# Kernel optimization log

Hardware: AMD Instinct MI355X
Metric: run time of the kernel (lower is better)

The kernel has to match this reference:

```python
import jax, jax.numpy as jnp
import numpy as np
import math

DIM = 2048
D_STATE = 64
EXPAND = 2
CHUNK = 64
HEADDIM = 64
D_CONV = 4
D_INNER = EXPAND * DIM          # 4096
NHEADS = D_INNER // HEADDIM     # 64


def _segsum(x):
    """x: (..., T) -> (..., T, T); out[i,j] = sum_{k=j+1}^{i} x[k] for i>=j else -inf."""
    T = x.shape[-1]
    keep = jnp.tril(jnp.ones((T, T), bool), -1)          # strictly lower
    seg = jnp.cumsum(jnp.where(keep, x[..., None], 0.0), axis=-2)
    valid = jnp.tril(jnp.ones((T, T), bool))
    return jnp.where(valid, seg, -jnp.inf)


def _ssd(X, A, B, C, block):
    """Chunkwise SSD scan (Mamba-2 Listing 1). X:(b,L,h,p) A:(b,L,h) B,C:(b,L,h,n)."""
    b, L, h, p = X.shape
    n = B.shape[-1]
    c = L // block
    X = X.reshape(b, c, block, h, p)
    A = A.reshape(b, c, block, h)
    B = B.reshape(b, c, block, h, n)
    C = C.reshape(b, c, block, h, n)
    A = jnp.transpose(A, (0, 3, 1, 2))                    # (b,h,c,l)
    A_cum = jnp.cumsum(A, axis=-1)
    # intra-chunk (diagonal block) output
    L_intra = jnp.exp(_segsum(A))                         # (b,h,c,l,s)
    Y_diag = jnp.einsum('bclhn,bcshn,bhcls,bcshp->bclhp', C, B, L_intra, X)
    # per-chunk final states
    decay_states = jnp.exp(A_cum[..., -1:] - A_cum)       # (b,h,c,l)
    states = jnp.einsum('bclhn,bhcl,bclhp->bchpn', B, decay_states, X)
    states = jnp.concatenate([jnp.zeros_like(states[:, :1]), states], axis=1)
    # inter-chunk recurrence across chunk boundaries
    chunk_end = jnp.pad(A_cum[..., -1], ((0, 0), (0, 0), (1, 0)))  # (b,h,c+1)
    decay_chunk = jnp.exp(_segsum(chunk_end))             # (b,h,c+1,c+1)
    new_states = jnp.einsum('bhzc,bchpn->bzhpn', decay_chunk, states)
    states_per_chunk = new_states[:, :-1]
    # off-diagonal contribution from carried-in states
    state_decay_out = jnp.exp(A_cum)                      # (b,h,c,l)
    Y_off = jnp.einsum('bclhn,bchpn,bhcl->bclhp', C, states_per_chunk, state_decay_out)
    return (Y_diag + Y_off).reshape(b, L, h, p)


def setup_inputs() -> dict:
    key = jax.random.key(0)
    ks = jax.random.split(key, 6)
    b, l = 2, 2048
    x = jax.random.normal(ks[0], (b, l, DIM), jnp.float32)
    proj_out = 2 * D_INNER + 2 * D_STATE + NHEADS
    in_proj_w = jax.random.normal(ks[1], (proj_out, DIM), jnp.float32) / math.sqrt(DIM)
    conv_w = jax.random.normal(ks[2], (D_INNER, 1, D_CONV), jnp.float32) / math.sqrt(D_CONV)
    conv_b = jnp.zeros((D_INNER,), jnp.float32)
    out_proj_w = jax.random.normal(ks[3], (DIM, D_INNER), jnp.float32) / math.sqrt(D_INNER)
    A_log = jnp.zeros((NHEADS,), jnp.float32)
    D_skip = jnp.ones((D_INNER,), jnp.float32)
    u = jax.random.uniform(ks[4], (NHEADS,), jnp.float32)
    dt = jnp.clip(jnp.exp(u * (math.log(0.1) - math.log(0.001)) + math.log(0.001)), 1e-4, None)
    dt_bias = dt + jnp.log(-jnp.expm1(-dt))
    return dict(x=x, in_proj_w=in_proj_w, conv_w=conv_w, conv_b=conv_b,
                out_proj_w=out_proj_w, A_log=A_log, D_skip=D_skip, dt_bias=dt_bias)


def reference(x, in_proj_w, conv_w, conv_b, out_proj_w, A_log, D_skip, dt_bias):
    b, l, _ = x.shape
    proj = x @ in_proj_w.T
    splits = [D_INNER, 2 * D_INNER, 2 * D_INNER + D_STATE, 2 * D_INNER + 2 * D_STATE]
    x_branch, z, B_in, C_in, dt = jnp.split(proj, splits, axis=-1)
    # causal depthwise conv1d (torch pads both sides then slices [:l] == left-pad only)
    xc = jnp.transpose(x_branch, (0, 2, 1))               # (b, d_inner, l)
    xc = jax.lax.conv_general_dilated(
        xc, conv_w, (1,), [(D_CONV - 1, 0)],
        dimension_numbers=('NCH', 'OIH', 'NCH'), feature_group_count=D_INNER)
    xc = xc + conv_b[None, :, None]
    x_act = jax.nn.silu(jnp.transpose(xc, (0, 2, 1)))     # (b,l,d_inner)
    x_h = x_act.reshape(b, l, NHEADS, HEADDIM)
    dt_f = jax.nn.softplus(dt + dt_bias)                  # (b,l,h)
    A_f = -jnp.exp(A_log)                                 # (h,)
    X_disc = x_h * dt_f[..., None]
    A_disc = A_f[None, None, :] * dt_f
    B_b = jnp.broadcast_to(B_in[:, :, None, :], (b, l, NHEADS, D_STATE))
    C_b = jnp.broadcast_to(C_in[:, :, None, :], (b, l, NHEADS, D_STATE))
    Y = _ssd(X_disc, A_disc, B_b, C_b, CHUNK)             # (b,l,h,p)
    y = Y.reshape(b, l, D_INNER) + D_skip * x_act
    y = y * jax.nn.silu(z)
    return y @ out_proj_w.T
```

## Files before the change

kernel.cpp:

```cpp
#include <hip/hip_runtime.h>

typedef unsigned short u16;
typedef unsigned int   u32;
typedef __attribute__((ext_vector_type(8))) short bf16x8;
typedef __attribute__((ext_vector_type(4))) float f32x4;

__device__ __forceinline__ u16 f2bf(float f){
  u32 u = __builtin_bit_cast(u32, f);
  u32 r = (u + 0x7FFFu + ((u >> 16) & 1u)) >> 16;
  return (u16)r;
}
__device__ __forceinline__ float bf2f(u16 h){
  u32 u = ((u32)h) << 16;
  return __builtin_bit_cast(float, u);
}
__device__ __forceinline__ void llds16(const u16* g, u16* l){
  __builtin_amdgcn_global_load_lds((const __attribute__((address_space(1))) void*)g,
                                   (__attribute__((address_space(3))) void*)l, 16, 0, 0);
}

__global__ __launch_bounds__(256) void cast4(const float* __restrict__ in, u16* __restrict__ out, int n4){
  int i = blockIdx.x * 256 + threadIdx.x;
  if (i >= n4) return;
  float4 v = ((const float4*)in)[i];
  u32 lo = (u32)f2bf(v.x) | ((u32)f2bf(v.y) << 16);
  u32 hi = (u32)f2bf(v.z) | ((u32)f2bf(v.w) << 16);
  ((uint2*)out)[i] = make_uint2(lo, hi);
}

__global__ __launch_bounds__(256) void castpad_w1(const float* __restrict__ in, u16* __restrict__ out){
  int i = blockIdx.x * 256 + threadIdx.x;
  if (i >= 8448 * 512) return;
  int nrow = i >> 9;
  float4 v = make_float4(0.f, 0.f, 0.f, 0.f);
  if (nrow < 8384) v = ((const float4*)in)[i];
  u32 lo = (u32)f2bf(v.x) | ((u32)f2bf(v.y) << 16);
  u32 hi = (u32)f2bf(v.z) | ((u32)f2bf(v.w) << 16);
  ((uint2*)out)[i] = make_uint2(lo, hi);
}

template<bool OUTF32>
__global__ __launch_bounds__(256)
void gemm128(const u16* __restrict__ A, const u16* __restrict__ Bm, void* __restrict__ Cout,
             int NYT, int N, int K)
{
  __shared__ u16 As[8192], Bs[8192];
  const int tid = threadIdx.x;
  const int lane = tid & 63, wave = tid >> 6;
  const int wm = (wave >> 1) * 64, wn = (wave & 1) * 64;
  const int lr = lane & 15, lk8 = (lane >> 4) * 8;
  const int lterm = lr * 32 + (lk8 ^ ((lr & 8) << 1));
  const int nwg = gridDim.x;
  const int lid = blockIdx.x;
  const int q = nwg >> 3;
  const int swz = (lid & 7) * q + (lid >> 3);
  const int ty = swz % NYT, tx = swz / NYT;
  const size_t bm0 = (size_t)ty * 128;
  const size_t bn0 = (size_t)tx * 128;
  const int cg = (lane & 3) ^ ((lane & 32) ? 2 : 0);
  const int rsub = lane >> 2;
  const int ag0 = (wave >> 1) * 8;
  const int bg0 = (wave & 1) * 8;

  f32x4 acc[4][4] = {};

  for (int k0 = 0; k0 < K; k0 += 64) {
    __syncthreads();
    #pragma unroll
    for (int u = 0; u < 4; u++) {
      const int si = wave * 4 + u;
      const int row = (si >> 1) * 16 + rsub;
      const int kc = (si & 1) * 32 + cg * 8;
      llds16(A  + (bm0 + row) * (size_t)K + k0 + kc, As + si * 512 + lane * 8);
      llds16(Bm + (bn0 + row) * (size_t)K + k0 + kc, Bs + si * 512 + lane * 8);
    }
    __syncthreads();
    #pragma unroll
    for (int kb = 0; kb < 2; kb++) {
      bf16x8 af[4], bfv[4];
      #pragma unroll
      for (int m = 0; m < 4; m++) af[m]  = *(const bf16x8*)&As[(ag0 + m * 2 + kb) * 512 + lterm];
      #pragma unroll
      for (int n = 0; n < 4; n++) bfv[n] = *(const bf16x8*)&Bs[(bg0 + n * 2 + kb) * 512 + lterm];
      #pragma unroll
      for (int m = 0; m < 4; m++)
        #pragma unroll
        for (int n = 0; n < 4; n++)
          acc[m][n] = __builtin_amdgcn_mfma_f32_16x16x32_bf16(af[m], bfv[n], acc[m][n], 0, 0, 0);
    }
  }

  const int lg = (lane >> 4) * 4;
  #pragma unroll
  for (int m = 0; m < 4; m++)
    #pragma unroll
    for (int n = 0; n < 4; n++) {
      size_t col = bn0 + wn + n * 16 + lr;
      #pragma unroll
      for (int j = 0; j < 4; j++) {
        size_t row = bm0 + wm + m * 16 + lg + j;
        float v = acc[m][n][j];
        if (OUTF32) ((float*)Cout)[row * N + col] = v;
        else        ((u16*)Cout)[row * N + col] = f2bf(v);
      }
    }
}

__global__ __launch_bounds__(256)
void postproj(const u16* __restrict__ proj, const float* __restrict__ dt_bias,
              float* __restrict__ dtf, u16* __restrict__ Bb, u16* __restrict__ Cb)
{
  int i = blockIdx.x * 256 + threadIdx.x;
  if (i >= 4096 * 64) return;
  int bl = i >> 6, hh = i & 63;
  const u16* pr = proj + (size_t)bl * 8448;
  float dv = bf2f(pr[8320 + hh]) + dt_bias[hh];
  dtf[i] = dv > 20.f ? dv : log1pf(__expf(dv));
  Bb[i] = pr[8192 + hh];
  Cb[i] = pr[8256 + hh];
}

__global__ __launch_bounds__(256)
void conv_silu(const u16* __restrict__ proj, const float* __restrict__ cw,
               const float* __restrict__ cb, const float* __restrict__ dtf,
               u16* __restrict__ xact, u16* __restrict__ Xd)
{
  const int g = blockIdx.x;
  const int bl0 = g * 4;
  const int l0 = bl0 & 2047;
  const int d0 = blockIdx.y * 2048 + threadIdx.x * 8;
  const int hd = d0 >> 6;
  float4 wv[8];
  #pragma unroll
  for (int e = 0; e < 8; e++) wv[e] = *(const float4*)&cw[(size_t)(d0 + e) * 4];
  float bias[8];
  {
    float4 b0 = *(const float4*)&cb[d0];
    float4 b1 = *(const float4*)&cb[d0 + 4];
    bias[0]=b0.x; bias[1]=b0.y; bias[2]=b0.z; bias[3]=b0.w;
    bias[4]=b1.x; bias[5]=b1.y; bias[6]=b1.z; bias[7]=b1.w;
  }
  float r[7][8];
  #pragma unroll
  for (int t = 0; t < 7; t++) {
    const int l = l0 - 3 + t;
    if (l >= 0) {
      uint4 rv = *(const uint4*)(proj + (size_t)(bl0 - 3 + t) * 8448 + d0);
      const u16* re = (const u16*)&rv;
      #pragma unroll
      for (int e = 0; e < 8; e++) r[t][e] = bf2f(re[e]);
    } else {
      #pragma unroll
      for (int e = 0; e < 8; e++) r[t][e] = 0.f;
    }
  }
  #pragma unroll
  for (int lo = 0; lo < 4; lo++) {
    const float dt = dtf[(size_t)(bl0 + lo) * 64 + hd];
    u16 xo[8], xdo[8];
    #pragma unroll
    for (int e = 0; e < 8; e++) {
      float v = bias[e] + wv[e].x * r[lo][e] + wv[e].y * r[lo + 1][e]
                        + wv[e].z * r[lo + 2][e] + wv[e].w * r[lo + 3][e];
      float sil = v / (1.f + __expf(-v));
      xo[e]  = f2bf(sil);
      xdo[e] = f2bf(sil * dt);
    }
    *(uint4*)(xact + (size_t)(bl0 + lo) * 4096 + d0) = *(const uint4*)xo;
    *(uint4*)(Xd   + (size_t)(bl0 + lo) * 4096 + d0) = *(const uint4*)xdo;
  }
}

__global__ __launch_bounds__(256)
void ssd_states(const u16* __restrict__ Xd, const u16* __restrict__ Bg,
                const float* __restrict__ dtf, const float* __restrict__ A_log,
                u16* __restrict__ Stg, float* __restrict__ dtot)
{
  const int wg = blockIdx.x;
  const int b = wg >> 11, h = wg & 63;
  const int c = (wg >> 6) & 31;
  const int bl0 = b * 2048 + c * 64;
  __shared__ u16 Bt[64*64], Xts[64*64];
  __shared__ float avals[64], Acum[64], Adec[64];
  const int tid = threadIdx.x, wave = tid >> 6, lane = tid & 63;
  const int qi = (wave >> 1) * 32, qj = (wave & 1) * 32;
  const int lr = lane & 15, lk8 = (lane >> 4) * 8, lg = (lane >> 4) * 4;
  const float negA = -__expf(A_log[h]);

  if (tid < 64) avals[tid] = negA * dtf[(size_t)(bl0 + tid) * 64 + h];
  __syncthreads();
  if (tid < 64) { float s = 0.f; for (int j = 0; j <= tid; j++) s += avals[j]; Acum[tid] = s; }
  __syncthreads();
  if (tid < 64) Adec[tid] = __expf(Acum[63] - Acum[tid]);
  if (tid == 0) dtot[wg] = __expf(Acum[63]);
  __syncthreads();
  {
    int s = tid & 63, c0 = (tid >> 6) * 16;
    float dec = Adec[s];
    const u16* bs = Bg + (size_t)(bl0 + s) * 64 + c0;
    const u16* xs = Xd + (size_t)(bl0 + s) * 4096 + h * 64 + c0;
    #pragma unroll
    for (int j = 0; j < 16; j++) {
      Bt[(c0 + j) * 64 + s] = bs[j];
      Xts[(c0 + j) * 64 + s] = f2bf(bf2f(xs[j]) * dec);
    }
  }
  __syncthreads();
  f32x4 accst[2][2] = {};
  #pragma unroll
  for (int kk = 0; kk < 64; kk += 32) {
    bf16x8 xsf[2], btf[2];
    #pragma unroll
    for (int t = 0; t < 2; t++) {
      xsf[t] = *(const bf16x8*)&Xts[(qi + t * 16 + lr) * 64 + kk + lk8];
      btf[t] = *(const bf16x8*)&Bt [(qj + t * 16 + lr) * 64 + kk + lk8];
    }
    #pragma unroll
    for (int ti = 0; ti < 2; ti++)
      #pragma unroll
      for (int tj = 0; tj < 2; tj++)
        accst[ti][tj] = __builtin_amdgcn_mfma_f32_16x16x32_bf16(xsf[ti], btf[tj], accst[ti][tj], 0, 0, 0);
  }
  u16* So = Stg + (size_t)wg * 4096;
  #pragma unroll
  for (int ti = 0; ti < 2; ti++)
    #pragma unroll
    for (int tj = 0; tj < 2; tj++) {
      int nn = qj + tj * 16 + lr;
      #pragma unroll
      for (int r2 = 0; r2 < 4; r2++) {
        int pp = qi + ti * 16 + lg + r2;
        So[pp * 64 + nn] = f2bf(accst[ti][tj][r2]);
      }
    }
}

__global__ __launch_bounds__(256)
void ssd_scan(u16* __restrict__ Stg, const float* __restrict__ dtot)
{
  const int gid = blockIdx.x * 256 + threadIdx.x;
  const int bh = gid >> 12;
  const int pn = gid & 4095;
  const int b = bh >> 6, h = bh & 63;
  float R = 0.f;
  for (int c = 0; c < 32; ++c) {
    const int whc = b * 2048 + c * 64 + h;
    size_t idx = (size_t)whc * 4096 + pn;
    float st = bf2f(Stg[idx]);
    Stg[idx] = f2bf(R);
    R = R * dtot[whc] + st;
  }
}

__global__ __launch_bounds__(256)
void ssd_y(const u16* __restrict__ Xd, const u16* __restrict__ Bg, const u16* __restrict__ Cg,
           const float* __restrict__ dtf, const float* __restrict__ A_log,
           const u16* __restrict__ xact, const u16* __restrict__ proj,
           const float* __restrict__ Dskip, const u16* __restrict__ Stg,
           u16* __restrict__ Yout)
{
  const int wg = blockIdx.x;
  const int b = wg >> 11, h = wg & 63;
  const int c = (wg >> 6) & 31;
  const int bl0 = b * 2048 + c * 64;
  __shared__ u16 Cb[64*64], Bb[64*64], Xt[64*64], Sb[64*64], P[64*64];
  __shared__ float avals[64], Acum[64], Aexp[64];
  const int tid = threadIdx.x, wave = tid >> 6, lane = tid & 63;
  const int qi = (wave >> 1) * 32, qj = (wave & 1) * 32;
  const int lr = lane & 15, lk8 = (lane >> 4) * 8, lg = (lane >> 4) * 4;
  const float negA = -__expf(A_log[h]);

  if (tid < 64) avals[tid] = negA * dtf[(size_t)(bl0 + tid) * 64 + h];
  __syncthreads();
  if (tid < 64) { float s = 0.f; for (int j = 0; j <= tid; j++) s += avals[j]; Acum[tid] = s; }
  __syncthreads();
  if (tid < 64) Aexp[tid] = __expf(Acum[tid]);
  __syncthreads();
  {
    int l = tid >> 2, n0 = (tid & 3) * 16;
    const uint4* s0 = (const uint4*)(Cg + (size_t)(bl0 + l) * 64 + n0);
    *(uint4*)&Cb[l * 64 + n0] = s0[0]; *(uint4*)&Cb[l * 64 + n0 + 8] = s0[1];
    const uint4* s1 = (const uint4*)(Bg + (size_t)(bl0 + l) * 64 + n0);
    *(uint4*)&Bb[l * 64 + n0] = s1[0]; *(uint4*)&Bb[l * 64 + n0 + 8] = s1[1];
    int s = tid & 63, c0 = (tid >> 6) * 16;
    const u16* xs = Xd + (size_t)(bl0 + s) * 4096 + h * 64 + c0;
    #pragma unroll
    for (int j = 0; j < 16; j++) Xt[(c0 + j) * 64 + s] = xs[j];
    const uint4* sp = (const uint4*)(Stg + (size_t)wg * 4096 + tid * 16);
    *(uint4*)&Sb[tid * 16] = sp[0]; *(uint4*)&Sb[tid * 16 + 8] = sp[1];
  }
  __syncthreads();
  f32x4 accs[2][2] = {}; f32x4 accy[2][2] = {};
  #pragma unroll
  for (int kk = 0; kk < 64; kk += 32) {
    bf16x8 cf[2], bfr[2], sf[2];
    #pragma unroll
    for (int t = 0; t < 2; t++) {
      cf[t]  = *(const bf16x8*)&Cb[(qi + t * 16 + lr) * 64 + kk + lk8];
      bfr[t] = *(const bf16x8*)&Bb[(qj + t * 16 + lr) * 64 + kk + lk8];
      sf[t]  = *(const bf16x8*)&Sb[(qj + t * 16 + lr) * 64 + kk + lk8];
    }
    #pragma unroll
    for (int ti = 0; ti < 2; ti++)
      #pragma unroll
      for (int tj = 0; tj < 2; tj++) {
        accs[ti][tj] = __builtin_amdgcn_mfma_f32_16x16x32_bf16(cf[ti], bfr[tj], accs[ti][tj], 0, 0, 0);
        accy[ti][tj] = __builtin_amdgcn_mfma_f32_16x16x32_bf16(cf[ti], sf[tj],  accy[ti][tj], 0, 0, 0);
      }
  }
  #pragma unroll
  for (int ti = 0; ti < 2; ti++)
    #pragma unroll
    for (int tj = 0; tj < 2; tj++) {
      int j = qj + tj * 16 + lr;
      float Aj = Acum[j];
      #pragma unroll
      for (int r2 = 0; r2 < 4; r2++) {
        int i = qi + ti * 16 + lg + r2;
        float v = (i >= j) ? accs[ti][tj][r2] * __expf(Acum[i] - Aj) : 0.f;
        P[i * 64 + j] = f2bf(v);
        accy[ti][tj][r2] *= Aexp[i];
      }
    }
  __syncthreads();
  #pragma unroll
  for (int kk = 0; kk < 64; kk += 32) {
    bf16x8 pf[2], xf_[2];
    #pragma unroll
    for (int t = 0; t < 2; t++) {
      pf[t]  = *(const bf16x8*)&P [(qi + t * 16 + lr) * 64 + kk + lk8];
      xf_[t] = *(const bf16x8*)&Xt[(qj + t * 16 + lr) * 64 + kk + lk8];
    }
    #pragma unroll
    for (int ti = 0; ti < 2; ti++)
      #pragma unroll
      for (int tj = 0; tj < 2; tj++)
        accy[ti][tj] = __builtin_amdgcn_mfma_f32_16x16x32_bf16(pf[ti], xf_[tj], accy[ti][tj], 0, 0, 0);
  }
  #pragma unroll
  for (int ti = 0; ti < 2; ti++)
    #pragma unroll
    for (int tj = 0; tj < 2; tj++) {
      int pcol = qj + tj * 16 + lr;
      int d = h * 64 + pcol;
      float dsk = Dskip[d];
      #pragma unroll
      for (int r2 = 0; r2 < 4; r2++) {
        int lrow = qi + ti * 16 + lg + r2;
        size_t bl = (size_t)bl0 + lrow;
        float y = accy[ti][tj][r2];
        float xa = bf2f(xact[bl * 4096 + d]);
        float z = bf2f(proj[bl * 8448 + 4096 + d]);
        float sz = z / (1.f + __expf(-z));
        Yout[bl * 4096 + d] = f2bf((y + dsk * xa) * sz);
      }
    }
}

__global__ __launch_bounds__(256)
void ssd_kernel(const u16* __restrict__ Xd, const u16* __restrict__ Bg, const u16* __restrict__ Cg,
                const float* __restrict__ dtf, const float* __restrict__ A_log,
                const u16* __restrict__ xact, const u16* __restrict__ proj,
                const float* __restrict__ Dskip, u16* __restrict__ Yout)
{
  const int bh = blockIdx.x;
  const int b = bh >> 6, h = bh & 63;
  __shared__ float S[64 * 64];
  __shared__ u16 Cb[64*64], Bb[64*64], Bt[64*64], Xt[64*64], Xts[64*64], Sb[64*64], P[64*64];
  __shared__ float avals[64], Acum[64], Adec[64], Aexp[64];
  const int tid = threadIdx.x, wave = tid >> 6, lane = tid & 63;
  const int qi = (wave >> 1) * 32, qj = (wave & 1) * 32;
  const int lr = lane & 15, lk8 = (lane >> 4) * 8, lg = (lane >> 4) * 4;
  const float negA = -__expf(A_log[h]);

  for (int i = tid; i < 4096; i += 256) S[i] = 0.f;

  for (int c = 0; c < 32; ++c) {
    const int bl0 = b * 2048 + c * 64;
    __syncthreads();
    if (tid < 64) avals[tid] = negA * dtf[(size_t)(bl0 + tid) * 64 + h];
    __syncthreads();
    if (tid < 64) { float s = 0.f; for (int j = 0; j <= tid; j++) s += avals[j]; Acum[tid] = s; }
    __syncthreads();
    if (tid < 64) { float At = Acum[63]; Adec[tid] = __expf(At - Acum[tid]); Aexp[tid] = __expf(Acum[tid]); }
    __syncthreads();
    {
      int l = tid >> 2, n0 = (tid & 3) * 16;
      const uint4* s0 = (const uint4*)(Cg + (size_t)(bl0 + l) * 64 + n0);
      *(uint4*)&Cb[l * 64 + n0] = s0[0]; *(uint4*)&Cb[l * 64 + n0 + 8] = s0[1];
      const uint4* s1 = (const uint4*)(Bg + (size_t)(bl0 + l) * 64 + n0);
      *(uint4*)&Bb[l * 64 + n0] = s1[0]; *(uint4*)&Bb[l * 64 + n0 + 8] = s1[1];
      int s = tid & 63, c0 = (tid >> 6) * 16;
      float dec = Adec[s];
      const u16* bs = Bg + (size_t)(bl0 + s) * 64 + c0;
      const u16* xs = Xd + (size_t)(bl0 + s) * 4096 + h * 64 + c0;
      #pragma unroll
      for (int j = 0; j < 16; j++) {
        Bt[(c0 + j) * 64 + s] = bs[j];
        u16 xv = xs[j];
        Xt[(c0 + j) * 64 + s] = xv;
        Xts[(c0 + j) * 64 + s] = f2bf(bf2f(xv) * dec);
      }
      int p = tid >> 2, m0 = (tid & 3) * 16;
      #pragma unroll
      for (int j = 0; j < 16; j++) Sb[p * 64 + m0 + j] = f2bf(S[p * 64 + m0 + j]);
    }
    __syncthreads();
    f32x4 accs[2][2] = {}; f32x4 accy[2][2] = {};
    #pragma unroll
    for (int kk = 0; kk < 64; kk += 32) {
      bf16x8 cf[2], bfr[2], sf[2];
      #pragma unroll
      for (int t = 0; t < 2; t++) {
        cf[t]  = *(const bf16x8*)&Cb[(qi + t * 16 + lr) * 64 + kk + lk8];
        bfr[t] = *(const bf16x8*)&Bb[(qj + t * 16 + lr) * 64 + kk + lk8];
        sf[t]  = *(const bf16x8*)&Sb[(qj + t * 16 + lr) * 64 + kk + lk8];
      }
      #pragma unroll
      for (int ti = 0; ti < 2; ti++)
        #pragma unroll
        for (int tj = 0; tj < 2; tj++) {
          accs[ti][tj] = __builtin_amdgcn_mfma_f32_16x16x32_bf16(cf[ti], bfr[tj], accs[ti][tj], 0, 0, 0);
          accy[ti][tj] = __builtin_amdgcn_mfma_f32_16x16x32_bf16(cf[ti], sf[tj],  accy[ti][tj], 0, 0, 0);
        }
    }
    #pragma unroll
    for (int ti = 0; ti < 2; ti++)
      #pragma unroll
      for (int tj = 0; tj < 2; tj++) {
        int j = qj + tj * 16 + lr;
        float Aj = Acum[j];
        #pragma unroll
        for (int r2 = 0; r2 < 4; r2++) {
          int i = qi + ti * 16 + lg + r2;
          float v = (i >= j) ? accs[ti][tj][r2] * __expf(Acum[i] - Aj) : 0.f;
          P[i * 64 + j] = f2bf(v);
          accy[ti][tj][r2] *= Aexp[i];
        }
      }
    __syncthreads();
    f32x4 accst[2][2] = {};
    #pragma unroll
    for (int kk = 0; kk < 64; kk += 32) {
      bf16x8 pf[2], xf_[2], xsf[2], btf[2];
      #pragma unroll
      for (int t = 0; t < 2; t++) {
        pf[t]  = *(const bf16x8*)&P  [(qi + t * 16 + lr) * 64 + kk + lk8];
        xf_[t] = *(const bf16x8*)&Xt [(qj + t * 16 + lr) * 64 + kk + lk8];
        xsf[t] = *(const bf16x8*)&Xts[(qi + t * 16 + lr) * 64 + kk + lk8];
        btf[t] = *(const bf16x8*)&Bt [(qj + t * 16 + lr) * 64 + kk + lk8];
      }
      #pragma unroll
      for (int ti = 0; ti < 2; ti++)
        #pragma unroll
        for (int tj = 0; tj < 2; tj++) {
          accy[ti][tj]  = __builtin_amdgcn_mfma_f32_16x16x32_bf16(pf[ti],  xf_[tj], accy[ti][tj],  0, 0, 0);
          accst[ti][tj] = __builtin_amdgcn_mfma_f32_16x16x32_bf16(xsf[ti], btf[tj], accst[ti][tj], 0, 0, 0);
        }
    }
    float dtot = Aexp[63];
    #pragma unroll
    for (int ti = 0; ti < 2; ti++)
      #pragma unroll
      for (int tj = 0; tj < 2; tj++) {
        int nn = qj + tj * 16 + lr;
        #pragma unroll
        for (int r2 = 0; r2 < 4; r2++) {
          int pp = qi + ti * 16 + lg + r2;
          int idx = pp * 64 + nn;
          S[idx] = dtot * S[idx] + accst[ti][tj][r2];
        }
      }
    #pragma unroll
    for (int ti = 0; ti < 2; ti++)
      #pragma unroll
      for (int tj = 0; tj < 2; tj++) {
        int pcol = qj + tj * 16 + lr;
        int d = h * 64 + pcol;
        float dsk = Dskip[d];
        #pragma unroll
        for (int r2 = 0; r2 < 4; r2++) {
          int lrow = qi + ti * 16 + lg + r2;
          size_t bl = (size_t)bl0 + lrow;
          float y = accy[ti][tj][r2];
          float xa = bf2f(xact[bl * 4096 + d]);
          float z = bf2f(proj[bl * 8448 + 4096 + d]);
          float sz = z / (1.f + __expf(-z));
          Yout[bl * 4096 + d] = f2bf((y + dsk * xa) * sz);
        }
      }
  }
}

extern "C" void kernel_launch(void* const* d_in, const int* in_sizes, int n_in,
                              void* d_out, int out_size, void* d_ws, size_t ws_size,
                              hipStream_t stream) {
  const float* x    = (const float*)d_in[0];
  const float* w1   = (const float*)d_in[1];
  const float* cw   = (const float*)d_in[2];
  const float* cbv  = (const float*)d_in[3];
  const float* w2   = (const float*)d_in[4];
  const float* alog = (const float*)d_in[5];
  const float* dsk  = (const float*)d_in[6];
  const float* dtb  = (const float*)d_in[7];
  float* out = (float*)d_out;

  char* ws = (char*)d_ws;
  u16*  x_bf  = (u16*)(ws + 0);
  u16*  w1p   = (u16*)(ws + 16777216);
  u16*  w2b   = (u16*)(ws + 51380224);
  u16*  proj  = (u16*)(ws + 68157440);
  float* dtf  = (float*)(ws + 137363456);
  u16*  Bbf   = (u16*)(ws + 138412032);
  u16*  Cbf   = (u16*)(ws + 138936320);
  u16*  xact  = (u16*)(ws + 139460608);
  u16*  Xdd   = (u16*)(ws + 173015040);
  u16*  yin   = (u16*)(ws + 206569472);
  u16*  Stg   = (u16*)(ws + 240123904);
  float* dtot = (float*)(ws + 273678336);
  const size_t NEED_PAR = 273694720ull;

  cast4<<<8192, 256, 0, stream>>>(x,  x_bf, 2097152);
  castpad_w1<<<16896, 256, 0, stream>>>(w1, w1p);
  cast4<<<8192, 256, 0, stream>>>(w2, w2b, 2097152);

  gemm128<false><<<2112, 256, 0, stream>>>(x_bf, w1p, proj, 32, 8448, 2048);

  postproj<<<1024, 256, 0, stream>>>(proj, dtb, dtf, Bbf, Cbf);
  conv_silu<<<dim3(1024, 2), 256, 0, stream>>>(proj, cw, cbv, dtf, xact, Xdd);

  if (ws_size >= NEED_PAR) {
    ssd_states<<<4096, 256, 0, stream>>>(Xdd, Bbf, dtf, alog, Stg, dtot);
    ssd_scan<<<2048, 256, 0, stream>>>(Stg, dtot);
    ssd_y<<<4096, 256, 0, stream>>>(Xdd, Bbf, Cbf, dtf, alog, xact, proj, dsk, Stg, yin);
  } else {
    ssd_kernel<<<128, 256, 0, stream>>>(Xdd, Bbf, Cbf, dtf, alog, xact, proj, dsk, yin);
  }

  gemm128<true><<<512, 256, 0, stream>>>(yin, w2b, out, 32, 2048, 4096);
}
```

Measured before the change: 413.5 us.

## Split-K the output projection GEMM with a separate partial-sum reduction kernel

The output projection GEMM is split into two K halves. A new kernel writes each half's fp32 partial tile into the now-unused proj workspace region, and a second elementwise kernel adds the two partials into the output. This doubles the block count from 512 to 1024, giving the GPU more parallel work to fill its compute units. The cost is an extra kernel launch plus the writes and reads of two full fp32 partial matrices.

```diff
diff --git a/kernel.cpp b/kernel.cpp
--- a/kernel.cpp
+++ b/kernel.cpp
@@ -107,6 +107,81 @@
 }
 
 __global__ __launch_bounds__(256)
+void gemm128sk(const u16* __restrict__ A, const u16* __restrict__ Bm, float* __restrict__ P,
+               int NYT, int N, int KLEN, int LDK)
+{
+  __shared__ u16 As[8192], Bs[8192];
+  const int tid = threadIdx.x;
+  const int lane = tid & 63, wave = tid >> 6;
+  const int wm = (wave >> 1) * 64, wn = (wave & 1) * 64;
+  const int lr = lane & 15, lk8 = (lane >> 4) * 8;
+  const int lterm = lr * 32 + (lk8 ^ ((lr & 8) << 1));
+  const int lid = blockIdx.x;
+  const int ks = lid >> 9;
+  const int lid2 = lid & 511;
+  const int q = 512 >> 3;
+  const int swz = (lid2 & 7) * q + (lid2 >> 3);
+  const int ty = swz % NYT, tx = swz / NYT;
+  const size_t bm0 = (size_t)ty * 128;
+  const size_t bn0 = (size_t)tx * 128;
+  const size_t koff = (size_t)ks * KLEN;
+  float* Pout = P + (size_t)ks * 8388608;
+  const int cg = (lane & 3) ^ ((lane & 32) ? 2 : 0);
+  const int rsub = lane >> 2;
+  const int ag0 = (wave >> 1) * 8;
+  const int bg0 = (wave & 1) * 8;
+
+  f32x4 acc[4][4] = {};
+
+  for (int k0 = 0; k0 < KLEN; k0 += 64) {
+    __syncthreads();
+    #pragma unroll
+    for (int u = 0; u < 4; u++) {
+      const int si = wave * 4 + u;
+      const int row = (si >> 1) * 16 + rsub;
+      const int kc = (si & 1) * 32 + cg * 8;
+      llds16(A  + (bm0 + row) * (size_t)LDK + koff + k0 + kc, As + si * 512 + lane * 8);
+      llds16(Bm + (bn0 + row) * (size_t)LDK + koff + k0 + kc, Bs + si * 512 + lane * 8);
+    }
+    __syncthreads();
+    #pragma unroll
+    for (int kb = 0; kb < 2; kb++) {
+      bf16x8 af[4], bfv[4];
+      #pragma unroll
+      for (int m = 0; m < 4; m++) af[m]  = *(const bf16x8*)&As[(ag0 + m * 2 + kb) * 512 + lterm];
+      #pragma unroll
+      for (int n = 0; n < 4; n++) bfv[n] = *(const bf16x8*)&Bs[(bg0 + n * 2 + kb) * 512 + lterm];
+      #pragma unroll
+      for (int m = 0; m < 4; m++)
+        #pragma unroll
+        for (int n = 0; n < 4; n++)
+          acc[m][n] = __builtin_amdgcn_mfma_f32_16x16x32_bf16(af[m], bfv[n], acc[m][n], 0, 0, 0);
+    }
+  }
+
+  const int lg = (lane >> 4) * 4;
+  #pragma unroll
+  for (int m = 0; m < 4; m++)
+    #pragma unroll
+    for (int n = 0; n < 4; n++) {
+      size_t col = bn0 + wn + n * 16 + lr;
+      #pragma unroll
+      for (int j = 0; j < 4; j++) {
+        size_t row = bm0 + wm + m * 16 + lg + j;
+        Pout[row * N + col] = acc[m][n][j];
+      }
+    }
+}
+
+__global__ __launch_bounds__(256)
+void addp(const float* __restrict__ p0, const float* __restrict__ p1, float* __restrict__ out){
+  int i = blockIdx.x * 256 + threadIdx.x;
+  float4 a = ((const float4*)p0)[i];
+  float4 b = ((const float4*)p1)[i];
+  ((float4*)out)[i] = make_float4(a.x + b.x, a.y + b.y, a.z + b.z, a.w + b.w);
+}
+
+__global__ __launch_bounds__(256)
 void postproj(const u16* __restrict__ proj, const float* __restrict__ dt_bias,
               float* __restrict__ dtf, u16* __restrict__ Bb, u16* __restrict__ Cb)
 {
@@ -519,6 +594,8 @@
   u16*  Stg   = (u16*)(ws + 240123904);
   float* dtot = (float*)(ws + 273678336);
   const size_t NEED_PAR = 273694720ull;
+  float* p0 = (float*)(ws + 68157440);
+  float* p1 = p0 + 8388608;
 
   cast4<<<8192, 256, 0, stream>>>(x,  x_bf, 2097152);
   castpad_w1<<<16896, 256, 0, stream>>>(w1, w1p);
@@ -537,5 +614,6 @@
     ssd_kernel<<<128, 256, 0, stream>>>(Xdd, Bbf, Cbf, dtf, alog, xact, proj, dsk, yin);
   }
 
-  gemm128<true><<<512, 256, 0, stream>>>(yin, w2b, out, 32, 2048, 4096);
-}
+  gemm128sk<<<1024, 256, 0, stream>>>(yin, w2b, p0, 32, 2048, 2048, 4096);
+  addp<<<8192, 256, 0, stream>>>(p0, p1, out);
+}
```

Measured after the change: 436.7 us. 1.06x slower.
